# Optimization experiments

Hardware: AMD Instinct MI355X
Metric: run time of the kernel (lower is better)

Reference implementation:

```python
import jax, jax.numpy as jnp
import numpy as np

B, H, L, D = 4, 16, 4096, 64
EPS = 1e-6  # self.epsilon in LinearAttention


def setup_inputs() -> dict:
    key = jax.random.key(0)
    kq, kk, kv = jax.random.split(key, 3)
    q = jax.random.normal(kq, (B, H, L, D), dtype=jnp.float32)
    k = jax.random.normal(kk, (B, H, L, D), dtype=jnp.float32)
    v = jax.random.normal(kv, (B, H, L, D), dtype=jnp.float32)
    attention_mask = jnp.ones((B, L), dtype=jnp.float32)
    return {"q": q, "k": k, "v": v, "attention_mask": attention_mask}


def reference(q, k, v, attention_mask):
    # feature map: elu(x) + 1 (applied in compute_scores to q and k)
    qf = jax.nn.elu(q) + 1.0
    kf = jax.nn.elu(k) + 1.0
    # mask: attention_mask.unsqueeze(1).unsqueeze(-1) -> [B,1,L,1]
    m = attention_mask[:, None, :, None]
    kf = kf * m
    vm = v * m
    # causal path: per-position cumulative sums along sequence dim
    k_cumsum = jnp.cumsum(kf, axis=2)            # [B,H,L,D]
    kv_cumsum = jnp.cumsum(kf * vm, axis=2)      # [B,H,L,D] (diagonal kv state)
    z = jnp.sum(qf * k_cumsum, axis=-1) + EPS    # [B,H,L]
    z = z * attention_mask[:, None, :]
    out = (qf * kv_cumsum) / z[..., None]        # [B,H,L,D]
    return out
```

## Files before the change

### kernel.cpp

```cpp
#include <hip/hip_runtime.h>
#include <hip/hip_bf16.h>

namespace {

constexpr int Hh    = 16;
constexpr int LL    = 4096;
constexpr int DD    = 64;
constexpr int BH    = 64;
constexpr int CHUNK = 128;
constexpr int NCH   = LL / CHUNK;
constexpr int RPT   = 8;
constexpr int RECF  = 128;
constexpr float EPS = 1e-6f;

typedef __attribute__((ext_vector_type(4))) float f32x4;

__device__ __forceinline__ float elu1(float x) {
    return x > 0.0f ? x + 1.0f : __expf(x);
}

template<int CTRL>
__device__ __forceinline__ float dpp_xor_add(float x) {
    int yi = __builtin_amdgcn_update_dpp(0, __float_as_int(x), CTRL, 0xF, 0xF, true);
    return x + __int_as_float(yi);
}
template<int IMM>
__device__ __forceinline__ float swz_xor_add(float x) {
    int yi = __builtin_amdgcn_ds_swizzle(__float_as_int(x), IMM);
    return x + __int_as_float(yi);
}
__device__ __forceinline__ float team_sum16(float x) {
    x = dpp_xor_add<0xB1>(x);
    x = dpp_xor_add<0x4E>(x);
    x = swz_xor_add<0x101F>(x);
    x = swz_xor_add<0x201F>(x);
    return x;
}

__device__ __forceinline__ float4 f4add(float4 a, float4 b) {
    return make_float4(a.x + b.x, a.y + b.y, a.z + b.z, a.w + b.w);
}

__global__ __launch_bounds__(256) void la_pass1(
    const float* __restrict__ kp, const float* __restrict__ vp,
    const float* __restrict__ maskp, float* __restrict__ ws)
{
    const int blk  = blockIdx.x;
    const int bh   = blk >> 5;
    const int ch   = blk & (NCH - 1);
    const int b    = bh >> 4;
    const int t    = threadIdx.x;
    const int qd   = t & 15;
    const int team = t >> 4;

    const long base  = ((long)bh * LL + (long)ch * CHUNK) * DD;
    const long rbase = base + (long)team * RPT * DD + qd * 4;
    const float* mrow = maskp + (long)b * LL + (long)ch * CHUNK + team * RPT;

    float4 sk = make_float4(0.f, 0.f, 0.f, 0.f);
    float4 sv = make_float4(0.f, 0.f, 0.f, 0.f);

    #pragma unroll
    for (int r = 0; r < RPT; ++r) {
        const float4 k4 = *(const float4*)(kp + rbase + (long)r * DD);
        const float4 v4 = *(const float4*)(vp + rbase + (long)r * DD);
        const float  m  = mrow[r];
        const float kf0 = elu1(k4.x) * m;
        const float kf1 = elu1(k4.y) * m;
        const float kf2 = elu1(k4.z) * m;
        const float kf3 = elu1(k4.w) * m;
        sk.x += kf0;              sk.y += kf1;
        sk.z += kf2;              sk.w += kf3;
        sv.x += kf0 * (v4.x * m); sv.y += kf1 * (v4.y * m);
        sv.z += kf2 * (v4.z * m); sv.w += kf3 * (v4.w * m);
    }

    __shared__ float red[16][RECF];
    red[team][qd*4+0] = sk.x; red[team][qd*4+1] = sk.y;
    red[team][qd*4+2] = sk.z; red[team][qd*4+3] = sk.w;
    red[team][64+qd*4+0] = sv.x; red[team][64+qd*4+1] = sv.y;
    red[team][64+qd*4+2] = sv.z; red[team][64+qd*4+3] = sv.w;
    __syncthreads();

    if (t < RECF) {
        float acc = 0.f;
        #pragma unroll
        for (int i = 0; i < 16; ++i) acc += red[i][t];
        ws[((long)bh * NCH + ch) * RECF + t] = acc;
    }
}

__global__ __launch_bounds__(RECF) void la_scan(float* __restrict__ ws)
{
    const int bh = blockIdx.x;
    const int t  = threadIdx.x;
    float* wb = ws + (long)bh * NCH * RECF + t;

    float vals[NCH];
    #pragma unroll
    for (int c = 0; c < NCH; ++c) vals[c] = wb[(long)c * RECF];

    float acc = 0.f;
    #pragma unroll
    for (int c = 0; c < NCH; ++c) {
        const float x = vals[c];
        wb[(long)c * RECF] = acc;
        acc += x;
    }
}

__global__ __launch_bounds__(256, 4) void la_pass2(
    const float* __restrict__ qp, const float* __restrict__ kp,
    const float* __restrict__ vp, const float* __restrict__ maskp,
    const float* __restrict__ ws, float* __restrict__ outp)
{
    const int blk  = blockIdx.x;
    const int bh   = blk >> 5;
    const int ch   = blk & (NCH - 1);
    const int b    = bh >> 4;
    const int t    = threadIdx.x;
    const int qd   = t & 15;
    const int team = t >> 4;

    const long base  = ((long)bh * LL + (long)ch * CHUNK) * DD;
    const long rbase = base + (long)team * RPT * DD + qd * 4;
    const float* mrow = maskp + (long)b * LL + (long)ch * CHUNK + team * RPT;

    const float* rec = ws + ((long)bh * NCH + ch) * RECF;
    const float4 ck = *(const float4*)(rec + qd * 4);
    const float4 cv = *(const float4*)(rec + 64 + qd * 4);

    float4 kb[RPT], vb[RPT];
    float  mv[RPT];
    #pragma unroll
    for (int r = 0; r < RPT; ++r) {
        kb[r] = *(const float4*)(kp + rbase + (long)r * DD);
        vb[r] = *(const float4*)(vp + rbase + (long)r * DD);
        mv[r] = mrow[r];
    }

    #pragma unroll
    for (int r = 0; r < RPT; ++r) {
        const float m = mv[r];
        float4 f;
        f.x = elu1(kb[r].x) * m; f.y = elu1(kb[r].y) * m;
        f.z = elu1(kb[r].z) * m; f.w = elu1(kb[r].w) * m;
        float4 g;
        g.x = f.x * (vb[r].x * m); g.y = f.y * (vb[r].y * m);
        g.z = f.z * (vb[r].z * m); g.w = f.w * (vb[r].w * m);
        kb[r] = f;
        vb[r] = g;
    }

    float4 tk = make_float4(0.f, 0.f, 0.f, 0.f);
    float4 tv = make_float4(0.f, 0.f, 0.f, 0.f);
    #pragma unroll
    for (int r = 0; r < RPT; ++r) { tk = f4add(tk, kb[r]); tv = f4add(tv, vb[r]); }

    __shared__ float red[16][RECF];
    __shared__ float pre[16][RECF];
    red[team][qd*4+0] = tk.x; red[team][qd*4+1] = tk.y;
    red[team][qd*4+2] = tk.z; red[team][qd*4+3] = tk.w;
    red[team][64+qd*4+0] = tv.x; red[team][64+qd*4+1] = tv.y;
    red[team][64+qd*4+2] = tv.z; red[team][64+qd*4+3] = tv.w;

    float4 qb[RPT];
    #pragma unroll
    for (int r = 0; r < RPT; ++r)
        qb[r] = *(const float4*)(qp + rbase + (long)r * DD);

    __syncthreads();
    if (t < RECF) {
        float acc = 0.f;
        #pragma unroll
        for (int i = 0; i < 16; ++i) { pre[i][t] = acc; acc += red[i][t]; }
    }
    __syncthreads();

    float4 rk, rv;
    rk.x = ck.x + pre[team][qd*4+0]; rk.y = ck.y + pre[team][qd*4+1];
    rk.z = ck.z + pre[team][qd*4+2]; rk.w = ck.w + pre[team][qd*4+3];
    rv.x = cv.x + pre[team][64+qd*4+0]; rv.y = cv.y + pre[team][64+qd*4+1];
    rv.z = cv.z + pre[team][64+qd*4+2]; rv.w = cv.w + pre[team][64+qd*4+3];

    #pragma unroll
    for (int r = 0; r < RPT; ++r) {
        rk = f4add(rk, kb[r]);
        rv = f4add(rv, vb[r]);

        float4 qf;
        qf.x = elu1(qb[r].x); qf.y = elu1(qb[r].y);
        qf.z = elu1(qb[r].z); qf.w = elu1(qb[r].w);

        float pz = qf.x*rk.x + qf.y*rk.y + qf.z*rk.z + qf.w*rk.w;
        pz = team_sum16(pz);

        const float z   = (pz + EPS) * mv[r];
        const float inv = __builtin_amdgcn_rcpf(z);

        f32x4 o;
        o.x = qf.x * rv.x * inv;
        o.y = qf.y * rv.y * inv;
        o.z = qf.z * rv.z * inv;
        o.w = qf.w * rv.w * inv;
        __builtin_nontemporal_store(o, (f32x4*)(outp + rbase + (long)r * DD));
    }
}

}

extern "C" void kernel_launch(void* const* d_in, const int* in_sizes, int n_in,
                              void* d_out, int out_size, void* d_ws, size_t ws_size,
                              hipStream_t stream) {
    const float* q    = (const float*)d_in[0];
    const float* k    = (const float*)d_in[1];
    const float* v    = (const float*)d_in[2];
    const float* mask = (const float*)d_in[3];
    float* out = (float*)d_out;
    float* ws  = (float*)d_ws;

    la_pass1<<<dim3(BH * NCH), dim3(256), 0, stream>>>(k, v, mask, ws);
    la_scan <<<dim3(BH),       dim3(RECF), 0, stream>>>(ws);
    la_pass2<<<dim3(BH * NCH), dim3(256), 0, stream>>>(q, k, v, mask, ws, out);
}
```

Before: 67.09 us.

## Stage K/V tiles in LDS via direct global-to-LDS loads in pass2

Pass2 now loads the 128x64 K and V chunk tiles straight into shared memory with global_load_lds instead of holding them in registers. The elu feature map and k*v products are recomputed from LDS in both the chunk-sum loop and the scan loop. The prefix array is folded into the reduction buffer, and the occupancy hint of 4 blocks is dropped. The aim is to cut register pressure and use asynchronous DMA-style loads, at the cost of 64KB of LDS per block (which limits blocks per CU) and duplicated elu work.

```diff
diff --git a/kernel.cpp b/kernel.cpp
--- a/kernel.cpp
+++ b/kernel.cpp
@@ -1,5 +1,6 @@
 #include <hip/hip_runtime.h>
 #include <hip/hip_bf16.h>
+#include <stdint.h>
 
 namespace {
 
@@ -11,6 +12,7 @@
 constexpr int NCH   = LL / CHUNK;
 constexpr int RPT   = 8;
 constexpr int RECF  = 128;
+constexpr int TILEF = CHUNK * DD;
 constexpr float EPS = 1e-6f;
 
 typedef __attribute__((ext_vector_type(4))) float f32x4;
@@ -37,8 +39,10 @@
     return x;
 }
 
-__device__ __forceinline__ float4 f4add(float4 a, float4 b) {
-    return make_float4(a.x + b.x, a.y + b.y, a.z + b.z, a.w + b.w);
+typedef const __attribute__((address_space(1))) void* as1_t;
+typedef __attribute__((address_space(3))) void* as3_t;
+__device__ __forceinline__ void gload16(const void* g, void* l) {
+    __builtin_amdgcn_global_load_lds((as1_t)g, (as3_t)l, 16, 0, 0);
 }
 
 __global__ __launch_bounds__(256) void la_pass1(
@@ -109,7 +113,7 @@
     }
 }
 
-__global__ __launch_bounds__(256, 4) void la_pass2(
+__global__ __launch_bounds__(256) void la_pass2(
     const float* __restrict__ qp, const float* __restrict__ kp,
     const float* __restrict__ vp, const float* __restrict__ maskp,
     const float* __restrict__ ws, float* __restrict__ outp)
@@ -121,72 +125,97 @@
     const int t    = threadIdx.x;
     const int qd   = t & 15;
     const int team = t >> 4;
+    const int wave = t >> 6;
+    const int ln   = t & 63;
 
     const long base  = ((long)bh * LL + (long)ch * CHUNK) * DD;
     const long rbase = base + (long)team * RPT * DD + qd * 4;
     const float* mrow = maskp + (long)b * LL + (long)ch * CHUNK + team * RPT;
 
+    __shared__ __align__(16) float tileK[TILEF];
+    __shared__ __align__(16) float tileV[TILEF];
+    __shared__ float red[16][RECF];
+
+    {
+        const int woff = wave * 256;
+        #pragma unroll
+        for (int i = 0; i < 8; ++i)
+            gload16(kp + base + i * 1024 + woff + ln * 4, &tileK[i * 1024 + woff]);
+        #pragma unroll
+        for (int i = 0; i < 8; ++i)
+            gload16(vp + base + i * 1024 + woff + ln * 4, &tileV[i * 1024 + woff]);
+    }
+
     const float* rec = ws + ((long)bh * NCH + ch) * RECF;
     const float4 ck = *(const float4*)(rec + qd * 4);
     const float4 cv = *(const float4*)(rec + 64 + qd * 4);
 
-    float4 kb[RPT], vb[RPT];
-    float  mv[RPT];
-    #pragma unroll
-    for (int r = 0; r < RPT; ++r) {
-        kb[r] = *(const float4*)(kp + rbase + (long)r * DD);
-        vb[r] = *(const float4*)(vp + rbase + (long)r * DD);
-        mv[r] = mrow[r];
-    }
-
-    #pragma unroll
-    for (int r = 0; r < RPT; ++r) {
-        const float m = mv[r];
-        float4 f;
-        f.x = elu1(kb[r].x) * m; f.y = elu1(kb[r].y) * m;
-        f.z = elu1(kb[r].z) * m; f.w = elu1(kb[r].w) * m;
-        float4 g;
-        g.x = f.x * (vb[r].x * m); g.y = f.y * (vb[r].y * m);
-        g.z = f.z * (vb[r].z * m); g.w = f.w * (vb[r].w * m);
-        kb[r] = f;
-        vb[r] = g;
-    }
-
+    float mv[RPT];
+    #pragma unroll
+    for (int r = 0; r < RPT; ++r) mv[r] = mrow[r];
+
+    float4 qb[RPT];
+    #pragma unroll
+    for (int r = 0; r < RPT; ++r)
+        qb[r] = *(const float4*)(qp + rbase + (long)r * DD);
+
+    asm volatile("s_waitcnt vmcnt(0)" ::: "memory");
+    __syncthreads();
+
+    const int tbase = (team * RPT) * DD + qd * 4;
     float4 tk = make_float4(0.f, 0.f, 0.f, 0.f);
     float4 tv = make_float4(0.f, 0.f, 0.f, 0.f);
     #pragma unroll
-    for (int r = 0; r < RPT; ++r) { tk = f4add(tk, kb[r]); tv = f4add(tv, vb[r]); }
-
-    __shared__ float red[16][RECF];
-    __shared__ float pre[16][RECF];
+    for (int r = 0; r < RPT; ++r) {
+        const float4 k4 = *(const float4*)&tileK[tbase + r * DD];
+        const float4 v4 = *(const float4*)&tileV[tbase + r * DD];
+        const float  m  = mv[r];
+        const float kf0 = elu1(k4.x) * m;
+        const float kf1 = elu1(k4.y) * m;
+        const float kf2 = elu1(k4.z) * m;
+        const float kf3 = elu1(k4.w) * m;
+        tk.x += kf0;              tk.y += kf1;
+        tk.z += kf2;              tk.w += kf3;
+        tv.x += kf0 * (v4.x * m); tv.y += kf1 * (v4.y * m);
+        tv.z += kf2 * (v4.z * m); tv.w += kf3 * (v4.w * m);
+    }
+
     red[team][qd*4+0] = tk.x; red[team][qd*4+1] = tk.y;
     red[team][qd*4+2] = tk.z; red[team][qd*4+3] = tk.w;
     red[team][64+qd*4+0] = tv.x; red[team][64+qd*4+1] = tv.y;
     red[team][64+qd*4+2] = tv.z; red[team][64+qd*4+3] = tv.w;
-
-    float4 qb[RPT];
-    #pragma unroll
-    for (int r = 0; r < RPT; ++r)
-        qb[r] = *(const float4*)(qp + rbase + (long)r * DD);
-
-    __syncthreads();
+    __syncthreads();
+
     if (t < RECF) {
         float acc = 0.f;
         #pragma unroll
-        for (int i = 0; i < 16; ++i) { pre[i][t] = acc; acc += red[i][t]; }
+        for (int i = 0; i < 16; ++i) {
+            const float x = red[i][t];
+            red[i][t] = acc;
+            acc += x;
+        }
     }
     __syncthreads();
 
     float4 rk, rv;
-    rk.x = ck.x + pre[team][qd*4+0]; rk.y = ck.y + pre[team][qd*4+1];
-    rk.z = ck.z + pre[team][qd*4+2]; rk.w = ck.w + pre[team][qd*4+3];
-    rv.x = cv.x + pre[team][64+qd*4+0]; rv.y = cv.y + pre[team][64+qd*4+1];
-    rv.z = cv.z + pre[team][64+qd*4+2]; rv.w = cv.w + pre[team][64+qd*4+3];
+    rk.x = ck.x + red[team][qd*4+0]; rk.y = ck.y + red[team][qd*4+1];
+    rk.z = ck.z + red[team][qd*4+2]; rk.w = ck.w + red[team][qd*4+3];
+    rv.x = cv.x + red[team][64+qd*4+0]; rv.y = cv.y + red[team][64+qd*4+1];
+    rv.z = cv.z + red[team][64+qd*4+2]; rv.w = cv.w + red[team][64+qd*4+3];
 
     #pragma unroll
     for (int r = 0; r < RPT; ++r) {
-        rk = f4add(rk, kb[r]);
-        rv = f4add(rv, vb[r]);
+        const float4 k4 = *(const float4*)&tileK[tbase + r * DD];
+        const float4 v4 = *(const float4*)&tileV[tbase + r * DD];
+        const float  m  = mv[r];
+        const float kf0 = elu1(k4.x) * m;
+        const float kf1 = elu1(k4.y) * m;
+        const float kf2 = elu1(k4.z) * m;
+        const float kf3 = elu1(k4.w) * m;
+        rk.x += kf0;              rk.y += kf1;
+        rk.z += kf2;              rk.w += kf3;
+        rv.x += kf0 * (v4.x * m); rv.y += kf1 * (v4.y * m);
+        rv.z += kf2 * (v4.z * m); rv.w += kf3 * (v4.w * m);
 
         float4 qf;
         qf.x = elu1(qb[r].x); qf.y = elu1(qb[r].y);
@@ -195,7 +224,7 @@
         float pz = qf.x*rk.x + qf.y*rk.y + qf.z*rk.z + qf.w*rk.w;
         pz = team_sum16(pz);
 
-        const float z   = (pz + EPS) * mv[r];
+        const float z   = (pz + EPS) * m;
         const float inv = __builtin_amdgcn_rcpf(z);
 
         f32x4 o;
```

Result: no change. 66.02 us (-1.6%).
